# Kernel optimization log

Measured on AMD Instinct MI355X. Metric: run time of the kernel, lower is better.

## Reference

```python
import jax, jax.numpy as jnp
import numpy as np
import math

PHI = (1 + math.sqrt(5)) / 2
B, T, D, H = 2, 2048, 1024, 16
DH = D // H
DC = 1024
DFF = int(D * PHI)  # 1657


def setup_inputs() -> dict:
    key = jax.random.key(0)
    ks = jax.random.split(key, 16)
    n = lambda i, shape, s=0.02: jax.random.normal(ks[i], shape, jnp.float32) * s
    tril = jnp.tril(jnp.ones((T, T), bool))
    mask = jnp.where(tril, 0.0, -1e9).astype(jnp.float32)[None, None]  # causal additive
    return dict(
        x=jax.random.normal(ks[0], (B, T, D), jnp.float32),
        center_from_above=jax.random.normal(ks[1], (B, DC), jnp.float32),
        mask=mask,
        gate_w=n(2, (D, 1), 0.5), gate_b=jnp.zeros((1,), jnp.float32),
        cb_w=n(3, (DC, 1), 0.5),
        nf_g=jnp.ones((D,), jnp.float32), nf_b=jnp.zeros((D,), jnp.float32),
        wq=n(4, (D, D)), wk=n(5, (D, D)), wv=n(6, (D, D)), wo=n(7, (D, D)),
        phase=jnp.linspace(0.0, math.pi, H).astype(jnp.float32),
        nb_g=jnp.ones((D,), jnp.float32), nb_b=jnp.zeros((D,), jnp.float32),
        up_w=n(8, (D, DFF)), up_b=jnp.zeros((DFF,), jnp.float32),
        dn_w=n(9, (DFF, D)), dn_b=jnp.zeros((D,), jnp.float32),
        commit_w=n(10, (D, 1)), commit_b=jnp.zeros((1,), jnp.float32),
        cproj_w=n(11, (D, DC)), cproj_b=jnp.zeros((DC,), jnp.float32),
        bcast_w=n(12, (DC, D)), bcast_b=jnp.zeros((D,), jnp.float32),
    )


def _ln(x, g, b, eps=1e-5):
    m = x.mean(-1, keepdims=True)
    v = ((x - m) ** 2).mean(-1, keepdims=True)
    return (x - m) * jax.lax.rsqrt(v + eps) * g + b


def _forward(x, center_from_above, mask, gate_w, gate_b, cb_w, nf_g, nf_b,
             wq, wk, wv, wo, phase, nb_g, nb_b, up_w, up_b, dn_w, dn_b,
             commit_w, commit_b, cproj_w, cproj_b, bcast_w, bcast_b):
    # broadcast center from above into the field
    x = x + (center_from_above @ bcast_w + bcast_b)[:, None, :]
    # binary aperture with straight-through estimator
    logits = x @ gate_w + gate_b + (center_from_above @ cb_w)[:, None, :]  # (B,T,1)
    prob = jax.nn.sigmoid(logits)
    hard = (prob > 0.5).astype(x.dtype)
    gate = hard - jax.lax.stop_gradient(prob) + prob
    h = _ln(x, nf_g, nf_b)
    heads = lambda w: (h @ w).reshape(B, T, H, DH).transpose(0, 2, 1, 3)  # (B,H,T,DH)
    Q, K, V = heads(wq), heads(wk), heads(wv)
    half = DH // 2
    c = jnp.cos(phase)[None, :, None, None]
    s = jnp.sin(phase)[None, :, None, None]
    def rot(z):
        re, im = z[..., :half], z[..., half:]
        return jnp.concatenate([re * c - im * s, re * s + im * c], axis=-1)
    Q, K = rot(Q), rot(K)
    ge = gate[:, None]  # (B,1,T,1)
    Q = Q * ge
    K = K * ge
    scores = jnp.einsum('bhqd,bhkd->bhqk', Q, K) / math.sqrt(DH) + mask
    attn = jax.nn.softmax(scores, axis=-1)
    fo = jnp.einsum('bhqk,bhkd->bhqd', attn, V).transpose(0, 2, 1, 3).reshape(B, T, D)
    fo = (fo @ wo) * gate
    x = x + fo
    h2 = _ln(x, nb_g, nb_b)
    ff = jax.nn.gelu(h2 @ up_w + up_b, approximate=False) @ dn_w + dn_b
    center_pool = x.mean(axis=1)  # (B,D)
    commit = jax.nn.sigmoid(center_pool @ commit_w + commit_b)  # (B,1)
    x = x + commit[:, None, :] * gate * ff
    center = jnp.tanh(center_pool @ cproj_w + cproj_b)  # (B,DC)
    return x, center, gate, commit


def reference(x, center_from_above, mask, gate_w, gate_b, cb_w, nf_g, nf_b,
              wq, wk, wv, wo, phase, nb_g, nb_b, up_w, up_b, dn_w, dn_b,
              commit_w, commit_b, cproj_w, cproj_b, bcast_w, bcast_b):
    return _forward(x, center_from_above, mask, gate_w, gate_b, cb_w, nf_g, nf_b,
                    wq, wk, wv, wo, phase, nb_g, nb_b, up_w, up_b, dn_w, dn_b,
                    commit_w, commit_b, cproj_w, cproj_b, bcast_w, bcast_b)
```

## Files before the change

kernel.cpp:

```cpp
#include <hip/hip_runtime.h>
#include <math.h>

#define B_   2
#define T_   2048
#define D_   1024
#define H_   16
#define DH_  64
#define DC_  1024
#define DFF_ 1656
#define DFFP_ 1664
#define MTOT 4096
#define NELEM_X 4194304ull

typedef short s16x8 __attribute__((ext_vector_type(8)));
typedef unsigned short u16x4 __attribute__((ext_vector_type(4)));
typedef unsigned short u16x8 __attribute__((ext_vector_type(8)));
typedef float f32x4 __attribute__((ext_vector_type(4)));
typedef float f32x16 __attribute__((ext_vector_type(16)));
typedef unsigned short bfbits;

__device__ __forceinline__ bfbits f2bf(float f) {
  unsigned int u = __builtin_bit_cast(unsigned int, f);
  u += 0x7fffu + ((u >> 16) & 1u);
  return (bfbits)(u >> 16);
}
__device__ __forceinline__ float bf2f(bfbits b) {
  unsigned int u = ((unsigned int)b) << 16;
  return __builtin_bit_cast(float, u);
}

__device__ __forceinline__ float vexp2(float x) {
  float r;
  asm("v_exp_f32 %0, %1" : "=v"(r) : "v"(x));
  return r;
}
__device__ __forceinline__ unsigned pkbf(float lo, float hi) {
  unsigned r;
  asm("v_cvt_pk_bf16_f32 %0, %1, %2" : "=v"(r) : "v"(lo), "v"(hi));
  return r;
}

__device__ __forceinline__ void gload16(const void* g, void* l) {
  __builtin_amdgcn_global_load_lds(
      (__attribute__((address_space(1))) void*)g,
      (__attribute__((address_space(3))) void*)l, 16, 0, 0);
}

constexpr size_t OFF_X1   = 0;
constexpr size_t OFF_H    = OFF_X1 + 4ull*NELEM_X;
constexpr size_t OFF_Q    = OFF_H  + 2ull*NELEM_X;
constexpr size_t OFF_K    = OFF_Q  + 2ull*NELEM_X;
constexpr size_t OFF_VT   = OFF_K  + 2ull*NELEM_X;
constexpr size_t OFF_AO   = OFF_VT + 2ull*NELEM_X;
constexpr size_t OFF_X2   = OFF_AO + 2ull*NELEM_X;
constexpr size_t OFF_WQKV = OFF_X2 + 4ull*NELEM_X;
constexpr size_t OFF_WO   = OFF_WQKV + 3072ull*1024*2;
constexpr size_t OFF_WUP  = OFF_WO   + 1024ull*1024*2;
constexpr size_t OFF_WDN  = OFF_WUP  + 1664ull*1024*2;
constexpr size_t OFF_BVEC = OFF_WDN  + 1024ull*1664*2;
constexpr size_t OFF_CBV  = OFF_BVEC + 2048ull*4;
constexpr size_t OFF_GATE = OFF_CBV  + 256;
constexpr size_t OFF_PART = OFF_GATE + 4096ull*4;
constexpr size_t OFF_POOL = OFF_PART + 128ull*1024*4;
constexpr size_t OFF_CMT  = OFF_POOL + 2048ull*4;
constexpr size_t OFF_PM   = OFF_CMT  + 256;
constexpr size_t OFF_PL   = OFF_PM   + 512ull*1024;

#define JB(q,a,b,s) ((unsigned)(q) | ((unsigned)(a)<<8) | ((unsigned)(b)<<16) | ((unsigned)(s)<<24))
__constant__ unsigned JOBS2[68] = {
  JB(9,0,10,255),
  JB(10,0,10,0),  JB(11,0,10,2),  JB(12,0,10,4),  JB(13,0,10,6),
  JB(14,0,10,8),  JB(15,0,10,10), JB(16,0,10,12), JB(17,0,10,14),
  JB(18,0,10,16), JB(19,0,10,18), JB(20,0,10,20), JB(21,0,10,23),
  JB(22,0,10,26), JB(23,0,10,29), JB(24,0,10,32), JB(25,0,10,35),
  JB(26,0,10,38), JB(27,0,10,41), JB(28,0,10,44), JB(29,0,10,47),
  JB(30,0,10,50), JB(31,0,10,54),
  JB(19,10,20,19), JB(20,10,20,21), JB(21,10,20,24), JB(22,10,20,27),
  JB(23,10,20,30), JB(24,10,20,33), JB(25,10,20,36), JB(26,10,20,39),
  JB(27,10,20,42), JB(28,10,20,45), JB(29,10,20,48), JB(30,10,20,51),
  JB(31,10,20,55),
  JB(29,20,30,49), JB(30,20,30,52), JB(31,20,30,56),
  JB(8,0,9,255),  JB(18,10,19,17), JB(28,20,29,46),
  JB(7,0,8,255),  JB(17,10,18,15), JB(27,20,28,43),
  JB(6,0,7,255),  JB(16,10,17,13), JB(26,20,27,40),
  JB(5,0,6,255),  JB(15,10,16,11), JB(25,20,26,37),
  JB(4,0,5,255),  JB(14,10,15,9),  JB(24,20,25,34),
  JB(3,0,4,255),  JB(13,10,14,7),  JB(23,20,24,31),
  JB(2,0,3,255),  JB(12,10,13,5),  JB(22,20,23,28),
  JB(1,0,2,255),  JB(11,10,12,3),  JB(21,20,22,25), JB(31,30,32,57),
  JB(0,0,1,255),  JB(10,10,11,1),  JB(20,20,21,22), JB(30,30,31,53),
};

__global__ __launch_bounds__(256)
void transpose_all(const float* __restrict__ wq, const float* __restrict__ wk,
                   const float* __restrict__ wv, const float* __restrict__ wo,
                   const float* __restrict__ up, const float* __restrict__ dn,
                   char* __restrict__ ws) {
  const int bid = blockIdx.x;
  const float* src;
  bfbits* dst;
  int R, C, Rpad, Npad, gw, loc;
  if (bid < 4096) {
    R = C = Rpad = Npad = 1024; gw = 32;
    const int j = bid >> 10; loc = bid & 1023;
    src = (j == 0) ? wq : (j == 1) ? wk : (j == 2) ? wv : wo;
    dst = (j < 3) ? (bfbits*)(ws + OFF_WQKV) + (size_t)j * 1024 * 1024
                  : (bfbits*)(ws + OFF_WO);
  } else if (bid < 5760) {
    R = 1024; C = DFF_; Rpad = 1024; Npad = DFFP_; gw = 32; loc = bid - 4096;
    src = up; dst = (bfbits*)(ws + OFF_WUP);
  } else {
    R = DFF_; C = 1024; Rpad = DFFP_; Npad = 1024; gw = 52; loc = bid - 5760;
    src = dn; dst = (bfbits*)(ws + OFF_WDN);
  }
  const int kb = (loc % gw) * 32, nb = (loc / gw) * 32;
  __shared__ float tile[32][33];
  const int tx = threadIdx.x & 31, ty = threadIdx.x >> 5;
  for (int i = ty; i < 32; i += 8) {
    const int k = kb + i, n = nb + tx;
    tile[i][tx] = (k < R && n < C) ? src[(size_t)k * C + n] : 0.f;
  }
  __syncthreads();
  for (int i = ty; i < 32; i += 8) {
    const int n = nb + i, k = kb + tx;
    if (n < Npad && k < Rpad) dst[(size_t)n * Rpad + k] = f2bf(tile[tx][i]);
  }
}

__global__ __launch_bounds__(256)
void bvec_cb_kernel(const float* __restrict__ cfa, const float* __restrict__ bw,
                    const float* __restrict__ bb, const float* __restrict__ cbw,
                    float* __restrict__ bvec, float* __restrict__ cbv) {
  const int b = blockIdx.y;
  if (blockIdx.x == 32) {
    const int tid = threadIdx.x;
    float4 a = *(const float4*)(cfa + b * 1024 + tid * 4);
    float4 w = *(const float4*)(cbw + tid * 4);
    float s = a.x * w.x + a.y * w.y + a.z * w.z + a.w * w.w;
    #pragma unroll
    for (int o = 32; o > 0; o >>= 1) s += __shfl_xor(s, o);
    __shared__ float ls[4];
    if ((tid & 63) == 0) ls[tid >> 6] = s;
    __syncthreads();
    if (tid == 0) cbv[b] = ls[0] + ls[1] + ls[2] + ls[3];
    return;
  }
  const int dl = threadIdx.x & 31, cl = threadIdx.x >> 5;
  const int d = blockIdx.x * 32 + dl;
  const float* vb = cfa + b * 1024;
  float s = 0.f;
  #pragma unroll 4
  for (int c = cl; c < 1024; c += 8)
    s += vb[c] * bw[(size_t)c * 1024 + d];
  __shared__ float red[8][32];
  red[cl][dl] = s;
  __syncthreads();
  if (threadIdx.x < 32) {
    float t = 0.f;
    #pragma unroll
    for (int i = 0; i < 8; ++i) t += red[i][threadIdx.x];
    const int dd = blockIdx.x * 32 + threadIdx.x;
    bvec[b * 1024 + dd] = t + bb[dd];
  }
}

__global__ __launch_bounds__(256)
void gemv_t(const float* __restrict__ v, const float* __restrict__ w,
            const float* __restrict__ bias, float* __restrict__ out) {
  const int b = blockIdx.y;
  const int dl = threadIdx.x & 31, cl = threadIdx.x >> 5;
  const int d = blockIdx.x * 32 + dl;
  const float* vb = v + b * 1024;
  float s = 0.f;
  #pragma unroll 4
  for (int c = cl; c < 1024; c += 8)
    s += vb[c] * w[(size_t)c * 1024 + d];
  __shared__ float red[8][32];
  red[cl][dl] = s;
  __syncthreads();
  if (threadIdx.x < 32) {
    float t = 0.f;
    #pragma unroll
    for (int i = 0; i < 8; ++i) t += red[i][threadIdx.x];
    const int dd = blockIdx.x * 32 + threadIdx.x;
    out[b * 1024 + dd] = tanhf(t + bias[dd]);
  }
}

__device__ __forceinline__ void blockreduce3(float& a, float& b, float& c) {
  #pragma unroll
  for (int o = 32; o > 0; o >>= 1) {
    a += __shfl_xor(a, o);
    b += __shfl_xor(b, o);
    c += __shfl_xor(c, o);
  }
  __shared__ float ls[3][4];
  const int lane = threadIdx.x & 63, w = threadIdx.x >> 6;
  if (lane == 0) { ls[0][w] = a; ls[1][w] = b; ls[2][w] = c; }
  __syncthreads();
  a = ls[0][0] + ls[0][1] + ls[0][2] + ls[0][3];
  b = ls[1][0] + ls[1][1] + ls[1][2] + ls[1][3];
  c = ls[2][0] + ls[2][1] + ls[2][2] + ls[2][3];
}

__global__ __launch_bounds__(256)
void ln1_kernel(const float* __restrict__ x, const float* __restrict__ bvec,
                const float* __restrict__ cbv, const float* __restrict__ gw,
                const float* __restrict__ gb, const float* __restrict__ nfg,
                const float* __restrict__ nfb, float* __restrict__ x1,
                bfbits* __restrict__ h, float* __restrict__ gate_ws,
                float* __restrict__ gate_out) {
  const int m = blockIdx.x, tid = threadIdx.x, b = m >> 11;
  const size_t ro = (size_t)m * D_ + tid * 4;
  float4 xv = *(const float4*)(x + ro);
  float4 bv = *(const float4*)(bvec + b * D_ + tid * 4);
  float4 v;
  v.x = xv.x + bv.x; v.y = xv.y + bv.y; v.z = xv.z + bv.z; v.w = xv.w + bv.w;
  float4 g4 = *(const float4*)(gw + tid * 4);
  float s  = v.x + v.y + v.z + v.w;
  float s2 = v.x*v.x + v.y*v.y + v.z*v.z + v.w*v.w;
  float dg = v.x*g4.x + v.y*g4.y + v.z*g4.z + v.w*g4.w;
  blockreduce3(s, s2, dg);
  const float mean = s * (1.0f/1024.0f);
  const float var  = s2 * (1.0f/1024.0f) - mean*mean;
  const float rstd = rsqrtf(var + 1e-5f);
  if (tid == 0) {
    const float logits = dg + gb[0] + cbv[b];
    const float prob = 1.0f / (1.0f + expf(-logits));
    const float hard = prob > 0.5f ? 1.0f : 0.0f;
    const float gv = (hard - prob) + prob;
    gate_ws[m] = gv; gate_out[m] = gv;
  }
  *(float4*)(x1 + ro) = v;
  float4 gg = *(const float4*)(nfg + tid * 4);
  float4 b2 = *(const float4*)(nfb + tid * 4);
  u16x4 hv;
  hv[0] = f2bf((v.x - mean) * rstd * gg.x + b2.x);
  hv[1] = f2bf((v.y - mean) * rstd * gg.y + b2.y);
  hv[2] = f2bf((v.z - mean) * rstd * gg.z + b2.z);
  hv[3] = f2bf((v.w - mean) * rstd * gg.w + b2.w);
  *(u16x4*)(h + ro) = hv;
}

__global__ __launch_bounds__(256)
void ln2_kernel(const float* __restrict__ x2, const float* __restrict__ gptr,
                const float* __restrict__ bptr, bfbits* __restrict__ h2) {
  const int m = blockIdx.x, tid = threadIdx.x;
  const size_t ro = (size_t)m * D_ + tid * 4;
  float4 v = *(const float4*)(x2 + ro);
  float s  = v.x + v.y + v.z + v.w;
  float s2 = v.x*v.x + v.y*v.y + v.z*v.z + v.w*v.w;
  float d0 = 0.f;
  blockreduce3(s, s2, d0);
  const float mean = s * (1.0f/1024.0f);
  const float var  = s2 * (1.0f/1024.0f) - mean*mean;
  const float rstd = rsqrtf(var + 1e-5f);
  float4 gg = *(const float4*)(gptr + tid * 4);
  float4 b2 = *(const float4*)(bptr + tid * 4);
  u16x4 hv;
  hv[0] = f2bf((v.x - mean) * rstd * gg.x + b2.x);
  hv[1] = f2bf((v.y - mean) * rstd * gg.y + b2.y);
  hv[2] = f2bf((v.z - mean) * rstd * gg.z + b2.z);
  hv[3] = f2bf((v.w - mean) * rstd * gg.w + b2.w);
  *(u16x4*)(h2 + ro) = hv;
}

template <int EPI, int BM, int BK, int BN>
__global__ void __launch_bounds__(256, 2)
gemm_bt(const bfbits* __restrict__ A, int lda,
        const bfbits* __restrict__ Bt, int ldb, int K,
        const float* __restrict__ p0, const float* __restrict__ p1,
        const float* __restrict__ p2,
        float* __restrict__ fo0, const float* __restrict__ fo1,
        bfbits* __restrict__ bo0, bfbits* __restrict__ bo1,
        bfbits* __restrict__ bo2) {
  constexpr int MI = BM / 32;
  constexpr int NJ = BN / 32;
  constexpr int RCH = BK / 8;
  constexpr int NK = BK / 32;
  __shared__ bfbits Asl[2][BM * BK];
  __shared__ bfbits Bsl[2][BN * BK];
  const int tid = threadIdx.x;
  const int lane = tid & 63, wave = tid >> 6;
  const int g = lane >> 4, l15 = lane & 15;
  const int wr = wave >> 1, wc = wave & 1;
  const int m0 = blockIdx.y * BM, n0 = blockIdx.x * BN;

  auto stage = [&](int k0, int p) {
    #pragma unroll
    for (int i = 0; i < (BM * RCH) / 256; ++i) {
      const int c = i * 256 + tid;
      const int row = c / RCH;
      const int ko = ((c % RCH) ^ (row & (RCH - 1))) * 8;
      gload16(A + (size_t)(m0 + row) * lda + (k0 + ko),
              (char*)&Asl[p][0] + c * 16);
    }
    #pragma unroll
    for (int i = 0; i < (BN * RCH) / 256; ++i) {
      const int c = i * 256 + tid;
      const int row = c / RCH;
      const int ko = ((c % RCH) ^ (row & (RCH - 1))) * 8;
      gload16(Bt + (size_t)(n0 + row) * ldb + (k0 + ko),
              (char*)&Bsl[p][0] + c * 16);
    }
  };

  f32x4 acc[MI][NJ] = {};
  stage(0, 0);
  __syncthreads();

  int t = 0;
  for (int k0 = 0; k0 < K; k0 += BK, ++t) {
    const int p = t & 1;
    if (k0 + BK < K) stage(k0 + BK, p ^ 1);
    s16x8 af[NK][MI], bfr[NK][NJ];
    #pragma unroll
    for (int kk = 0; kk < NK; ++kk) {
      #pragma unroll
      for (int i = 0; i < MI; ++i) {
        const int row = wr * (MI * 16) + i * 16 + l15;
        af[kk][i] = *(const s16x8*)&Asl[p][row * BK + (((kk * 4 + g) ^ (row & (RCH - 1))) * 8)];
      }
      #pragma unroll
      for (int i = 0; i < NJ; ++i) {
        const int row = wc * (NJ * 16) + i * 16 + l15;
        bfr[kk][i] = *(const s16x8*)&Bsl[p][row * BK + (((kk * 4 + g) ^ (row & (RCH - 1))) * 8)];
      }
    }
    #pragma unroll
    for (int kk = 0; kk < NK; ++kk)
      #pragma unroll
      for (int i = 0; i < MI; ++i)
        #pragma unroll
        for (int j = 0; j < NJ; ++j)
          acc[i][j] = __builtin_amdgcn_mfma_f32_16x16x32_bf16(af[kk][i], bfr[kk][j], acc[i][j], 0, 0, 0);
    __syncthreads();
  }

  const int b = m0 >> 11;
  const int trow0 = (m0 & 2047) + wr * (MI * 16);

  if constexpr (EPI == 0) {
    const float* gate = p0;
    const float* phase = p1;
    const int ncol0 = n0 + wc * 64;
    const int section = ncol0 >> 10;
    const int hh = (ncol0 & 1023) >> 6;
    if (section == 2) {
      bfbits* vt = bo2;
      const size_t vhead = (size_t)(b * H_ + hh) * DH_ * T_;
      #pragma unroll
      for (int mi = 0; mi < MI; ++mi) {
        const int tb = trow0 + mi * 16 + g * 4;
        #pragma unroll
        for (int ni = 0; ni < NJ; ++ni) {
          const int dh = ni * 16 + l15;
          unsigned* dst32 = (unsigned*)&vt[vhead + (size_t)dh * T_ + tb];
          dst32[0] = pkbf(acc[mi][ni][0], acc[mi][ni][1]);
          dst32[1] = pkbf(acc[mi][ni][2], acc[mi][ni][3]);
        }
      }
    } else {
      const float cc = cosf(phase[hh]);
      const float ssn = sinf(phase[hh]);
      const float qs = (section == 0) ? 0.125f * 1.44269504088896341f : 1.0f;
      bfbits* dst = (section == 0) ? bo0 : bo1;
      const size_t head = (size_t)(b * H_ + hh) * T_ * DH_;
      #pragma unroll
      for (int mi = 0; mi < MI; ++mi) {
        const int tb = trow0 + mi * 16 + g * 4;
        float gv[4];
        #pragma unroll
        for (int r = 0; r < 4; ++r) gv[r] = gate[(size_t)b * T_ + tb + r] * qs;
        #pragma unroll
        for (int ni = 0; ni < 2; ++ni) {
          const int dh = ni * 16 + l15;
          #pragma unroll
          for (int r = 0; r < 4; ++r) {
            const float re = acc[mi][ni][r];
            const float im = acc[mi][ni + 2][r];
            const size_t idx = head + (size_t)(tb + r) * DH_ + dh;
            dst[idx]      = f2bf((re * cc - im * ssn) * gv[r]);
            dst[idx + 32] = f2bf((re * ssn + im * cc) * gv[r]);
          }
        }
      }
    }
  } else if constexpr (EPI == 1) {
    const float* gate = p0;
    const float* x1 = fo1;
    float* x2 = fo0;
    #pragma unroll
    for (int mi = 0; mi < MI; ++mi) {
      const int m = m0 + wr * (MI * 16) + mi * 16 + g * 4;
      float gv[4];
      #pragma unroll
      for (int r = 0; r < 4; ++r) gv[r] = gate[m + r];
      #pragma unroll
      for (int ni = 0; ni < NJ; ++ni) {
        const int n = n0 + wc * (NJ * 16) + ni * 16 + l15;
        #pragma unroll
        for (int r = 0; r < 4; ++r) {
          const size_t idx = (size_t)(m + r) * D_ + n;
          x2[idx] = x1[idx] + acc[mi][ni][r] * gv[r];
        }
      }
    }
  } else if constexpr (EPI == 2) {
    const float* upb = p0;
    bfbits* outm = bo0;
    #pragma unroll
    for (int mi = 0; mi < MI; ++mi) {
      const int m = m0 + wr * (MI * 16) + mi * 16 + g * 4;
      #pragma unroll
      for (int ni = 0; ni < NJ; ++ni) {
        const int n = n0 + wc * (NJ * 16) + ni * 16 + l15;
        const float bb = upb[n < DFF_ ? n : DFF_ - 1];
        #pragma unroll
        for (int r = 0; r < 4; ++r) {
          float v = acc[mi][ni][r] + bb;
          v = 0.5f * v * (1.0f + erff(v * 0.70710678118654752f));
          outm[(size_t)(m + r) * DFFP_ + n] = f2bf(v);
        }
      }
    }
  } else {
    const float* dnb = p0;
    const float* gate = p1;
    const float* cmt = p2;
    const float* x2 = fo1;
    float* outx = fo0;
    const float cb = cmt[b];
    #pragma unroll
    for (int mi = 0; mi < MI; ++mi) {
      const int m = m0 + wr * (MI * 16) + mi * 16 + g * 4;
      float kv[4];
      #pragma unroll
      for (int r = 0; r < 4; ++r) kv[r] = cb * gate[m + r];
      #pragma unroll
      for (int ni = 0; ni < NJ; ++ni) {
        const int n = n0 + wc * (NJ * 16) + ni * 16 + l15;
        const float bb = dnb[n];
        #pragma unroll
        for (int r = 0; r < 4; ++r) {
          const size_t idx = (size_t)(m + r) * D_ + n;
          outx[idx] = x2[idx] + kv[r] * (acc[mi][ni][r] + bb);
        }
      }
    }
  }
}

__global__ void __launch_bounds__(128, 3)
attn_kernel(const bfbits* __restrict__ Qb, const bfbits* __restrict__ Kb,
            const bfbits* __restrict__ Vt, bfbits* __restrict__ AO,
            float* __restrict__ pm, float* __restrict__ pl,
            bfbits* __restrict__ pO) {
  __shared__ bfbits Kl[64 * 64];
  __shared__ bfbits Vl[64 * 64];
  const int pid = blockIdx.x;
  const int bh = pid & 31;
  const unsigned job = JOBS2[pid >> 5];
  const int qt = job & 0xFF;
  const int t0 = (job >> 8) & 0xFF;
  const int t1 = (job >> 16) & 0xFF;
  const int js = job >> 24;
  const int qb0 = qt * 64;
  const int tid = threadIdx.x, lane = tid & 63, wq = tid >> 6;
  const int l31 = lane & 31, hi = lane >> 5;
  const int qw = qb0 + wq * 32;

  const bfbits* Qp = Qb + ((size_t)bh * T_ + qw) * DH_;
  const bfbits* Kp = Kb + (size_t)bh * T_ * DH_;
  const bfbits* Vp = Vt + (size_t)bh * DH_ * T_;

  s16x8 qf[4];
  #pragma unroll
  for (int mf = 0; mf < 4; ++mf)
    qf[mf] = *(const s16x8*)(Qp + l31 * DH_ + mf * 16 + hi * 8);

  f32x16 o0 = {}, o1 = {};
  float mrun = -INFINITY, lrun = 0.f;

  const bfbits* kg[4];
  const bfbits* vg[4];
  int cb_[4];
  #pragma unroll
  for (int i = 0; i < 4; ++i) {
    const int c = i * 128 + tid;
    const int row = c >> 3;
    const int sc = ((c & 7) ^ (row & 7)) * 8;
    kg[i] = Kp + row * DH_ + sc;
    vg[i] = Vp + (size_t)row * T_ + sc;
    cb_[i] = c * 16;
  }

  for (int t = t0; t < t1; ++t) {
    const int k0 = t << 6;
    #pragma unroll
    for (int i = 0; i < 4; ++i) {
      gload16(kg[i] + (size_t)k0 * DH_, (char*)&Kl[0] + cb_[i]);
      gload16(vg[i] + k0,               (char*)&Vl[0] + cb_[i]);
    }
    __syncthreads();
    f32x16 s0 = {}, s1 = {};
    __builtin_amdgcn_s_setprio(1);
    #pragma unroll
    for (int mf = 0; mf < 4; ++mf) {
      const int ch = ((mf * 2 + hi) ^ (l31 & 7)) * 8;
      const s16x8 ka  = *(const s16x8*)&Kl[l31 * 64 + ch];
      const s16x8 kb2 = *(const s16x8*)&Kl[(32 + l31) * 64 + ch];
      s0 = __builtin_amdgcn_mfma_f32_32x32x16_bf16(ka,  qf[mf], s0, 0, 0, 0);
      s1 = __builtin_amdgcn_mfma_f32_32x32x16_bf16(kb2, qf[mf], s1, 0, 0, 0);
    }
    __builtin_amdgcn_s_setprio(0);
    if (t == qt) {
      const int qd = wq * 32 + l31;
      #pragma unroll
      for (int r = 0; r < 16; ++r) {
        const int krow = (r & 3) + 8 * (r >> 2) + 4 * hi;
        if (krow > qd)      s0[r] = -1e9f;
        if (krow + 32 > qd) s1[r] = -1e9f;
      }
    }
    float red[8];
    #pragma unroll
    for (int i = 0; i < 8; ++i)
      red[i] = fmaxf(fmaxf(s0[i], s0[i + 8]), fmaxf(s1[i], s1[i + 8]));
    #pragma unroll
    for (int i = 0; i < 4; ++i) red[i] = fmaxf(red[i], red[i + 4]);
    float mx = fmaxf(fmaxf(red[0], red[1]), fmaxf(red[2], red[3]));
    mx = fmaxf(mx, __shfl_xor(mx, 32));
    const bool need = __any(mx > mrun + 8.f) != 0;
    const float mnew = need ? fmaxf(mrun, mx) : mrun;
    s0 = s0 - mnew;
    s1 = s1 - mnew;
    #pragma unroll
    for (int i = 0; i < 16; ++i) { s0[i] = vexp2(s0[i]); s1[i] = vexp2(s1[i]); }
    float sr[8];
    #pragma unroll
    for (int i = 0; i < 8; ++i)
      sr[i] = (s0[i] + s0[i + 8]) + (s1[i] + s1[i + 8]);
    #pragma unroll
    for (int i = 0; i < 4; ++i) sr[i] += sr[i + 4];
    float sum = (sr[0] + sr[1]) + (sr[2] + sr[3]);
    sum += __shfl_xor(sum, 32);
    if (need) {
      const float alpha = vexp2(mrun - mnew);
      mrun = mnew;
      lrun = lrun * alpha + sum;
      o0 *= alpha;
      o1 *= alpha;
    } else {
      lrun += sum;
    }
    #pragma unroll
    for (int mf = 0; mf < 4; ++mf) {
      const f32x16& s = (mf < 2) ? s0 : s1;
      const int r0 = (mf & 1) * 8;
      const unsigned A0 = pkbf(s[r0 + 0], s[r0 + 1]);
      const unsigned A1 = pkbf(s[r0 + 2], s[r0 + 3]);
      const unsigned B0 = pkbf(s[r0 + 4], s[r0 + 5]);
      const unsigned B1 = pkbf(s[r0 + 6], s[r0 + 7]);
      const unsigned x0 = (unsigned)__shfl_xor((int)(hi ? A0 : B0), 32);
      const unsigned x1 = (unsigned)__shfl_xor((int)(hi ? A1 : B1), 32);
      uint4 wv;
      wv.x = hi ? x0 : A0;
      wv.y = hi ? x1 : A1;
      wv.z = hi ? B0 : x0;
      wv.w = hi ? B1 : x1;
      const s16x8 pf = __builtin_bit_cast(s16x8, wv);
      const int ch = ((mf * 2 + hi) ^ (l31 & 7)) * 8;
      const s16x8 v0 = *(const s16x8*)&Vl[l31 * 64 + ch];
      const s16x8 v1 = *(const s16x8*)&Vl[(32 + l31) * 64 + ch];
      __builtin_amdgcn_s_setprio(1);
      o0 = __builtin_amdgcn_mfma_f32_32x32x16_bf16(v0, pf, o0, 0, 0, 0);
      o1 = __builtin_amdgcn_mfma_f32_32x32x16_bf16(v1, pf, o1, 0, 0, 0);
      __builtin_amdgcn_s_setprio(0);
    }
    __syncthreads();
  }

  if (js == 255) {
    const float inv = 1.0f / lrun;
    const int q = qw + l31;
    bfbits* dst = AO + ((size_t)(bh >> 4) * T_ + q) * D_ + (bh & 15) * DH_;
    #pragma unroll
    for (int rp = 0; rp < 8; ++rp) {
      const int dh = ((2 * rp) & 3) + 8 * (rp >> 1) + 4 * hi;
      *(unsigned*)(dst + dh)      = pkbf(o0[2 * rp] * inv, o0[2 * rp + 1] * inv);
      *(unsigned*)(dst + 32 + dh) = pkbf(o1[2 * rp] * inv, o1[2 * rp + 1] * inv);
    }
  } else {
    const int jid = bh * 58 + js;
    const int qloc = wq * 32 + l31;
    pm[jid * 64 + qloc] = mrun;
    pl[jid * 64 + qloc] = lrun;
    bfbits* po = pO + (size_t)jid * 4096 + qloc * 64;
    #pragma unroll
    for (int rp = 0; rp < 8; ++rp) {
      const int dh = ((2 * rp) & 3) + 8 * (rp >> 1) + 4 * hi;
      *(unsigned*)(po + dh)      = pkbf(o0[2 * rp], o0[2 * rp + 1]);
      *(unsigned*)(po + 32 + dh) = pkbf(o1[2 * rp], o1[2 * rp + 1]);
    }
  }
}

__global__ void __launch_bounds__(256)
attn_merge(const float* __restrict__ pm, const float* __restrict__ pl,
           const bfbits* __restrict__ pO, bfbits* __restrict__ AO) {
  __shared__ float evs[4][64];
  __shared__ float invs[64];
  const int u = blockIdx.x;
  const int qt = 10 + (u >> 5), bh = u & 31;
  const int tid = threadIdx.x;
  const int P = (qt + 10) / 10;
  const int pbase = (qt < 20) ? (qt - 10) * 2
                  : (qt < 30) ? 20 + (qt - 20) * 3
                              : 50 + (qt - 30) * 4;
  const int jb = bh * 58 + pbase;
  if (tid < 64) {
    const int q = tid;
    float mv[4];
    float m = -INFINITY;
    for (int p = 0; p < P; ++p) {
      mv[p] = pm[(jb + p) * 64 + q];
      m = fmaxf(m, mv[p]);
    }
    float l = 0.f;
    for (int p = 0; p < P; ++p) {
      const float e = vexp2(mv[p] - m);
      evs[p][q] = e;
      l += pl[(jb + p) * 64 + q] * e;
    }
    invs[q] = 1.0f / l;
  }
  __syncthreads();
  const int q = tid >> 2, dh0 = (tid & 3) * 16;
  float acc[16] = {};
  for (int p = 0; p < P; ++p) {
    const float e = evs[p][q];
    const bfbits* src = pO + (size_t)(jb + p) * 4096 + q * 64 + dh0;
    const u16x8 a = *(const u16x8*)src;
    const u16x8 b2 = *(const u16x8*)(src + 8);
    #pragma unroll
    for (int i = 0; i < 8; ++i) {
      acc[i]     += bf2f(a[i]) * e;
      acc[8 + i] += bf2f(b2[i]) * e;
    }
  }
  const float inv = invs[q];
  uint4 w0, w1;
  w0.x = pkbf(acc[0] * inv,  acc[1] * inv);
  w0.y = pkbf(acc[2] * inv,  acc[3] * inv);
  w0.z = pkbf(acc[4] * inv,  acc[5] * inv);
  w0.w = pkbf(acc[6] * inv,  acc[7] * inv);
  w1.x = pkbf(acc[8] * inv,  acc[9] * inv);
  w1.y = pkbf(acc[10] * inv, acc[11] * inv);
  w1.z = pkbf(acc[12] * inv, acc[13] * inv);
  w1.w = pkbf(acc[14] * inv, acc[15] * inv);
  const int b = bh >> 4, hh = bh & 15;
  bfbits* dst = AO + ((size_t)b * T_ + qt * 64 + q) * D_ + hh * DH_ + dh0;
  *(uint4*)dst = w0;
  *(uint4*)(dst + 8) = w1;
}

__global__ __launch_bounds__(256)
void pool_part(const float* __restrict__ x2, float* __restrict__ part) {
  const int s = blockIdx.x, b = blockIdx.y, tid = threadIdx.x;
  const float* base = x2 + ((size_t)b * T_ + s * 32) * D_ + tid * 4;
  float ax = 0, ay = 0, az = 0, aw = 0;
  #pragma unroll 4
  for (int t = 0; t < 32; ++t) {
    float4 v = *(const float4*)(base + (size_t)t * D_);
    ax += v.x; ay += v.y; az += v.z; aw += v.w;
  }
  float4 ov; ov.x = ax; ov.y = ay; ov.z = az; ov.w = aw;
  *(float4*)(part + (size_t)(b * 64 + s) * D_ + tid * 4) = ov;
}

__global__ __launch_bounds__(256)
void pool_fin_commit(const float* __restrict__ part, const float* __restrict__ cw,
                     const float* __restrict__ cb0, float* __restrict__ pool,
                     float* __restrict__ cmt, float* __restrict__ out_cmt) {
  const int b = blockIdx.x, tid = threadIdx.x;
  const int d0 = tid * 4;
  float ax = 0, ay = 0, az = 0, aw = 0;
  #pragma unroll 8
  for (int i = 0; i < 64; ++i) {
    float4 v = *(const float4*)(part + (size_t)(b * 64 + i) * D_ + d0);
    ax += v.x; ay += v.y; az += v.z; aw += v.w;
  }
  ax *= (1.0f / 2048.0f); ay *= (1.0f / 2048.0f);
  az *= (1.0f / 2048.0f); aw *= (1.0f / 2048.0f);
  float4 ov; ov.x = ax; ov.y = ay; ov.z = az; ov.w = aw;
  *(float4*)(pool + b * 1024 + d0) = ov;
  float4 w = *(const float4*)(cw + d0);
  float s = ax * w.x + ay * w.y + az * w.z + aw * w.w;
  #pragma unroll
  for (int o = 32; o > 0; o >>= 1) s += __shfl_xor(s, o);
  __shared__ float ls[4];
  if ((tid & 63) == 0) ls[tid >> 6] = s;
  __syncthreads();
  if (tid == 0) {
    const float t = ls[0] + ls[1] + ls[2] + ls[3] + cb0[0];
    const float v = 1.0f / (1.0f + expf(-t));
    cmt[b] = v; out_cmt[b] = v;
  }
}

extern "C" void kernel_launch(void* const* d_in, const int* in_sizes, int n_in,
                              void* d_out, int out_size, void* d_ws, size_t ws_size,
                              hipStream_t stream) {
  (void)in_sizes; (void)n_in; (void)out_size; (void)ws_size;
  const float* x       = (const float*)d_in[0];
  const float* cfa     = (const float*)d_in[1];
  const float* gate_w  = (const float*)d_in[3];
  const float* gate_b  = (const float*)d_in[4];
  const float* cb_w    = (const float*)d_in[5];
  const float* nf_g    = (const float*)d_in[6];
  const float* nf_b    = (const float*)d_in[7];
  const float* wq      = (const float*)d_in[8];
  const float* wk      = (const float*)d_in[9];
  const float* wv      = (const float*)d_in[10];
  const float* wo      = (const float*)d_in[11];
  const float* phase   = (const float*)d_in[12];
  const float* nb_g    = (const float*)d_in[13];
  const float* nb_b    = (const float*)d_in[14];
  const float* up_w    = (const float*)d_in[15];
  const float* up_b    = (const float*)d_in[16];
  const float* dn_w    = (const float*)d_in[17];
  const float* dn_b    = (const float*)d_in[18];
  const float* cmt_w   = (const float*)d_in[19];
  const float* cmt_b   = (const float*)d_in[20];
  const float* cproj_w = (const float*)d_in[21];
  const float* cproj_b = (const float*)d_in[22];
  const float* bcast_w = (const float*)d_in[23];
  const float* bcast_b = (const float*)d_in[24];

  char* ws = (char*)d_ws;
  float*  x1     = (float*)(ws + OFF_X1);
  bfbits* h      = (bfbits*)(ws + OFF_H);
  bfbits* h2     = (bfbits*)(ws + OFF_H);
  bfbits* qb     = (bfbits*)(ws + OFF_Q);
  bfbits* kb     = (bfbits*)(ws + OFF_K);
  bfbits* vt     = (bfbits*)(ws + OFF_VT);
  bfbits* ffmid  = (bfbits*)(ws + OFF_Q);
  bfbits* ao     = (bfbits*)(ws + OFF_AO);
  float*  x2     = (float*)(ws + OFF_X2);
  bfbits* pO     = (bfbits*)(ws + OFF_X2);
  bfbits* wqkv_t = (bfbits*)(ws + OFF_WQKV);
  bfbits* wo_t   = (bfbits*)(ws + OFF_WO);
  bfbits* wup_t  = (bfbits*)(ws + OFF_WUP);
  bfbits* wdn_t  = (bfbits*)(ws + OFF_WDN);
  float*  bvec   = (float*)(ws + OFF_BVEC);
  float*  cbv    = (float*)(ws + OFF_CBV);
  float*  gate   = (float*)(ws + OFF_GATE);
  float*  part   = (float*)(ws + OFF_PART);
  float*  pool   = (float*)(ws + OFF_POOL);
  float*  cmt    = (float*)(ws + OFF_CMT);
  float*  pm     = (float*)(ws + OFF_PM);
  float*  pl     = (float*)(ws + OFF_PL);

  float* outx   = (float*)d_out;
  float* outc   = outx + NELEM_X;
  float* outg   = outc + B_ * DC_;
  float* outcmt = outg + B_ * T_;

  transpose_all<<<7424, 256, 0, stream>>>(wq, wk, wv, wo, up_w, dn_w, ws);

  bvec_cb_kernel<<<dim3(33, B_), 256, 0, stream>>>(cfa, bcast_w, bcast_b, cb_w,
                                                   bvec, cbv);

  ln1_kernel<<<MTOT, 256, 0, stream>>>(x, bvec, cbv, gate_w, gate_b, nf_g, nf_b,
                                       x1, h, gate, outg);

  gemm_bt<0, 128, 32, 128><<<dim3(24, 32), 256, 0, stream>>>(
      h, 1024, wqkv_t, 1024, 1024, gate, phase, nullptr,
      nullptr, nullptr, qb, kb, vt);

  attn_kernel<<<2176, 128, 0, stream>>>(qb, kb, vt, ao, pm, pl, pO);
  attn_merge<<<704, 256, 0, stream>>>(pm, pl, pO, ao);

  gemm_bt<1, 64, 64, 64><<<dim3(16, 64), 256, 0, stream>>>(
      ao, 1024, wo_t, 1024, 1024, gate, nullptr, nullptr,
      x2, x1, nullptr, nullptr, nullptr);

  ln2_kernel<<<MTOT, 256, 0, stream>>>(x2, nb_g, nb_b, h2);

  pool_part<<<dim3(64, B_), 256, 0, stream>>>(x2, part);
  pool_fin_commit<<<B_, 256, 0, stream>>>(part, cmt_w, cmt_b, pool, cmt, outcmt);
  gemv_t<<<dim3(32, B_), 256, 0, stream>>>(pool, cproj_w, cproj_b, outc);

  gemm_bt<2, 64, 64, 64><<<dim3(26, 64), 256, 0, stream>>>(
      h2, 1024, wup_t, 1024, 1024, up_b, nullptr, nullptr,
      nullptr, nullptr, ffmid, nullptr, nullptr);

  gemm_bt<3, 64, 64, 64><<<dim3(16, 64), 256, 0, stream>>>(
      ffmid, DFFP_, wdn_t, DFFP_, DFFP_, dn_b, gate, cmt,
      outx, x2, nullptr, nullptr, nullptr);
}
```

Baseline: 216.9 us.

## Give each attention wave private K/V LDS tiles and drop block barriers

Each of the two waves in the attention block now loads its own full copy of the K and V tiles into separate LDS buffers. This lets the kernel replace the block-wide __syncthreads with per-wave waitcnt instructions, and the V wait is deferred until after QK^T and softmax so the V load overlaps that compute. In exchange, LDS use and global/L2 traffic for K/V double per block, and each wave issues twice as many loads. Correctness depends on direct-to-LDS loads being complete and visible within the wave after vmcnt reaches zero.

```diff
diff --git a/kernel.cpp b/kernel.cpp
--- a/kernel.cpp
+++ b/kernel.cpp
@@ -456,8 +456,8 @@
             const bfbits* __restrict__ Vt, bfbits* __restrict__ AO,
             float* __restrict__ pm, float* __restrict__ pl,
             bfbits* __restrict__ pO) {
-  __shared__ bfbits Kl[64 * 64];
-  __shared__ bfbits Vl[64 * 64];
+  __shared__ bfbits Kl[2][64 * 64];
+  __shared__ bfbits Vl[2][64 * 64];
   const int pid = blockIdx.x;
   const int bh = pid & 31;
   const unsigned job = JOBS2[pid >> 5];
@@ -473,6 +473,8 @@
   const bfbits* Qp = Qb + ((size_t)bh * T_ + qw) * DH_;
   const bfbits* Kp = Kb + (size_t)bh * T_ * DH_;
   const bfbits* Vp = Vt + (size_t)bh * DH_ * T_;
+  bfbits* myK = &Kl[wq][0];
+  bfbits* myV = &Vl[wq][0];
 
   s16x8 qf[4];
   #pragma unroll
@@ -482,34 +484,30 @@
   f32x16 o0 = {}, o1 = {};
   float mrun = -INFINITY, lrun = 0.f;
 
-  const bfbits* kg[4];
-  const bfbits* vg[4];
-  int cb_[4];
-  #pragma unroll
-  for (int i = 0; i < 4; ++i) {
-    const int c = i * 128 + tid;
-    const int row = c >> 3;
-    const int sc = ((c & 7) ^ (row & 7)) * 8;
-    kg[i] = Kp + row * DH_ + sc;
-    vg[i] = Vp + (size_t)row * T_ + sc;
-    cb_[i] = c * 16;
-  }
-
   for (int t = t0; t < t1; ++t) {
     const int k0 = t << 6;
     #pragma unroll
-    for (int i = 0; i < 4; ++i) {
-      gload16(kg[i] + (size_t)k0 * DH_, (char*)&Kl[0] + cb_[i]);
-      gload16(vg[i] + k0,               (char*)&Vl[0] + cb_[i]);
-    }
-    __syncthreads();
+    for (int i = 0; i < 8; ++i) {
+      const int c = i * 64 + lane;
+      const int row = c >> 3;
+      const int sc = ((c & 7) ^ (row & 7)) * 8;
+      gload16(Kp + (size_t)(k0 + row) * DH_ + sc, (char*)myK + c * 16);
+    }
+    #pragma unroll
+    for (int i = 0; i < 8; ++i) {
+      const int c = i * 64 + lane;
+      const int row = c >> 3;
+      const int sc = ((c & 7) ^ (row & 7)) * 8;
+      gload16(Vp + (size_t)row * T_ + (k0 + sc), (char*)myV + c * 16);
+    }
+    asm volatile("s_waitcnt vmcnt(8)" ::: "memory");
     f32x16 s0 = {}, s1 = {};
     __builtin_amdgcn_s_setprio(1);
     #pragma unroll
     for (int mf = 0; mf < 4; ++mf) {
       const int ch = ((mf * 2 + hi) ^ (l31 & 7)) * 8;
-      const s16x8 ka  = *(const s16x8*)&Kl[l31 * 64 + ch];
-      const s16x8 kb2 = *(const s16x8*)&Kl[(32 + l31) * 64 + ch];
+      const s16x8 ka  = *(const s16x8*)&myK[l31 * 64 + ch];
+      const s16x8 kb2 = *(const s16x8*)&myK[(32 + l31) * 64 + ch];
       s0 = __builtin_amdgcn_mfma_f32_32x32x16_bf16(ka,  qf[mf], s0, 0, 0, 0);
       s1 = __builtin_amdgcn_mfma_f32_32x32x16_bf16(kb2, qf[mf], s1, 0, 0, 0);
     }
@@ -554,6 +552,7 @@
     } else {
       lrun += sum;
     }
+    asm volatile("s_waitcnt vmcnt(0)" ::: "memory");
     #pragma unroll
     for (int mf = 0; mf < 4; ++mf) {
       const f32x16& s = (mf < 2) ? s0 : s1;
@@ -571,14 +570,14 @@
       wv.w = hi ? B1 : x1;
       const s16x8 pf = __builtin_bit_cast(s16x8, wv);
       const int ch = ((mf * 2 + hi) ^ (l31 & 7)) * 8;
-      const s16x8 v0 = *(const s16x8*)&Vl[l31 * 64 + ch];
-      const s16x8 v1 = *(const s16x8*)&Vl[(32 + l31) * 64 + ch];
+      const s16x8 v0 = *(const s16x8*)&myV[l31 * 64 + ch];
+      const s16x8 v1 = *(const s16x8*)&myV[(32 + l31) * 64 + ch];
       __builtin_amdgcn_s_setprio(1);
       o0 = __builtin_amdgcn_mfma_f32_32x32x16_bf16(v0, pf, o0, 0, 0, 0);
       o1 = __builtin_amdgcn_mfma_f32_32x32x16_bf16(v1, pf, o1, 0, 0, 0);
       __builtin_amdgcn_s_setprio(0);
     }
-    __syncthreads();
+    asm volatile("s_waitcnt lgkmcnt(0)" ::: "memory");
   }
 
   if (js == 255) {
```

Result: slower. 229.8 us (+5.9%).
